# Kernel optimization log

Hardware: AMD Instinct MI355X
Metric: run time of the kernel (lower is better)

The kernel has to match this reference:

```python
import jax, jax.numpy as jnp
import numpy as np

EMBED_DIM = 1024
HEAD_SIZE = 64
BATCH = 8
SEQ = 2048


def setup_inputs() -> dict:
    key = jax.random.key(0)
    k1, k2, k3, k4 = jax.random.split(key, 4)
    x = jax.random.normal(k1, (BATCH, SEQ, EMBED_DIM), dtype=jnp.float32)
    # Dense(use_bias=False) kernels: [in, out]
    scale = 1.0 / np.sqrt(EMBED_DIM)
    Wq = jax.random.normal(k2, (EMBED_DIM, HEAD_SIZE), dtype=jnp.float32) * scale
    Wk = jax.random.normal(k3, (EMBED_DIM, HEAD_SIZE), dtype=jnp.float32) * scale
    Wv = jax.random.normal(k4, (EMBED_DIM, HEAD_SIZE), dtype=jnp.float32) * scale
    return {"x": x, "Wq": Wq, "Wk": Wk, "Wv": Wv}


def reference(x, Wq, Wk, Wv):
    B, S, E = x.shape
    q = jnp.einsum("bse,eh->bsh", x, Wq)
    k = jnp.einsum("bse,eh->bsh", x, Wk)
    v = jnp.einsum("bse,eh->bsh", x, Wv)
    # scores scaled by embedding_dim**-0.5 (as in the original code)
    w = jnp.einsum("bqh,bkh->bqk", q, k) * (E ** -0.5)
    causal = jnp.tril(jnp.ones((S, S), dtype=bool))  # True on/below diag
    w = jnp.where(causal, w, -jnp.inf)
    w = jax.nn.softmax(w, axis=-1)
    # dropout is identity at inference
    return jnp.einsum("bqk,bkh->bqh", w, v)
```

## Files before the change

### kernel.cpp

```cpp
#include <hip/hip_runtime.h>
#include <hip/hip_bf16.h>


#define BATCH 8
#define SEQ   2048
#define EMB   1024
#define HD    64
#define ROWS  (BATCH*SEQ)
#define NTOT  192
#define BK    64
#define NKT   (EMB / BK)

typedef __attribute__((ext_vector_type(8))) short short8;
typedef __attribute__((ext_vector_type(4))) float floatx4;

static __device__ __forceinline__ short f2bf(float f) {
  union { __hip_bfloat16 h; short s; } u;
  u.h = __float2bfloat16(f);
  return u.s;
}

static __device__ __forceinline__ short8 pack8(float4 u, float4 v) {
  short8 r;
  r[0] = f2bf(u.x); r[1] = f2bf(u.y); r[2] = f2bf(u.z); r[3] = f2bf(u.w);
  r[4] = f2bf(v.x); r[5] = f2bf(v.y); r[6] = f2bf(v.z); r[7] = f2bf(v.w);
  return r;
}

static __device__ __forceinline__ void gload_lds16(const void* g, void* l) {
  __builtin_amdgcn_global_load_lds(
      (const __attribute__((address_space(1))) unsigned int*)g,
      (__attribute__((address_space(3))) unsigned int*)l, 16, 0, 0);
}

__global__ __launch_bounds__(256) void wt_kernel(
    const float* __restrict__ Wq, const float* __restrict__ Wk,
    const float* __restrict__ Wv, short* __restrict__ Wts) {
  const int id = blockIdx.x * 256 + threadIdx.x;
  const int kt = id / 1536;
  const int rem = id - kt * 1536;
  const int np = rem >> 3;
  const int s = rem & 7;
  const float* __restrict__ W = (np < 64) ? Wq : ((np < 128) ? Wk : Wv);
  const int n = np & 63;
  const int k0 = kt * BK + (s ^ (np & 7)) * 8;
  short8 o;
#pragma unroll
  for (int u = 0; u < 8; ++u) o[u] = f2bf(W[(size_t)(k0 + u) * HD + n]);
  *(short8*)(Wts + (size_t)id * 8) = o;
}

__global__ __launch_bounds__(256, 2) void proj_kernel(
    const float* __restrict__ x, const short* __restrict__ Wts,
    short* __restrict__ qb, short* __restrict__ kb_, short* __restrict__ vtb) {
  __shared__ __align__(16) float As[32 * 64];
  __shared__ __align__(16) short Bs[192 * 64];

  const int t = threadIdx.x, lane = t & 63, w = t >> 6;
  const int lo = lane & 15, quad = lane >> 4;
  const int e = lo & 7;
  const int m0 = blockIdx.x * 32;

  const int cc0 = w * 2, cc1 = cc0 + 1;
  const int ar0 = cc0 * 4 + (lane >> 4);
  const int ar1 = cc1 * 4 + (lane >> 4);
  const int aj = lane & 15;
  const float* agp0 = x + (size_t)(m0 + ar0) * EMB + ((aj ^ (ar0 & 7)) * 4);
  const float* agp1 = x + (size_t)(m0 + ar1) * EMB + ((aj ^ (ar1 & 7)) * 4);
  float* alp0 = As + cc0 * 256;
  float* alp1 = As + cc1 * 256;

  const short* bgp = Wts + (size_t)(w * 6) * 512 + lane * 8;
  short* blp = Bs + (w * 6) * 512;

  floatx4 acc[2][3];
#pragma unroll
  for (int mf = 0; mf < 2; ++mf)
#pragma unroll
    for (int j = 0; j < 3; ++j) acc[mf][j] = (floatx4){0.f, 0.f, 0.f, 0.f};

  for (int kt = 0; kt < NKT; ++kt) {
    __syncthreads();
    gload_lds16(agp0 + kt * BK, alp0);
    gload_lds16(agp1 + kt * BK, alp1);
    const short* bg = bgp + (size_t)kt * 12288;
#pragma unroll
    for (int i = 0; i < 6; ++i)
      gload_lds16(bg + i * 512, blp + i * 512);
    __syncthreads();

    short8 af[2][2];
#pragma unroll
    for (int mf = 0; mf < 2; ++mf) {
      const float* Ar = As + (mf * 16 + lo) * 64;
#pragma unroll
      for (int ks = 0; ks < 2; ++ks) {
        const float4 f0 = *(const float4*)(Ar + (((8 * ks + 2 * quad) ^ e) << 2));
        const float4 f1 = *(const float4*)(Ar + (((8 * ks + 2 * quad + 1) ^ e) << 2));
        af[mf][ks] = pack8(f0, f1);
      }
    }
    short8 bf[3][2];
#pragma unroll
    for (int j = 0; j < 3; ++j) {
      const short* Br = Bs + ((w * 3 + j) * 16 + lo) * 64;
#pragma unroll
      for (int ks = 0; ks < 2; ++ks)
        bf[j][ks] = *(const short8*)(Br + (((4 * ks + quad) ^ e) << 3));
    }
#pragma unroll
    for (int ks = 0; ks < 2; ++ks)
#pragma unroll
      for (int j = 0; j < 3; ++j) {
        acc[0][j] = __builtin_amdgcn_mfma_f32_16x16x32_bf16(af[0][ks], bf[j][ks], acc[0][j], 0, 0, 0);
        acc[1][j] = __builtin_amdgcn_mfma_f32_16x16x32_bf16(af[1][ks], bf[j][ks], acc[1][j], 0, 0, 0);
      }
  }

  const int bb = m0 >> 11;
  const int sbase = (m0 & (SEQ - 1)) + quad * 4;
#pragma unroll
  for (int mf = 0; mf < 2; ++mf) {
    const int rowb = m0 + mf * 16 + quad * 4;
#pragma unroll
    for (int j = 0; j < 3; ++j) {
      const int nt = w * 3 + j;
      const floatx4 v = acc[mf][j];
      if (nt < 4) {
#pragma unroll
        for (int r = 0; r < 4; ++r)
          qb[(size_t)(rowb + r) * HD + nt * 16 + lo] = f2bf(v[r] * 0.03125f);
      } else if (nt < 8) {
#pragma unroll
        for (int r = 0; r < 4; ++r)
          kb_[(size_t)(rowb + r) * HD + (nt - 4) * 16 + lo] = f2bf(v[r]);
      } else {
        const int col = (nt - 8) * 16 + lo;
        short4 sv = make_short4(f2bf(v[0]), f2bf(v[1]), f2bf(v[2]), f2bf(v[3]));
        *(short4*)(vtb + ((size_t)bb * HD + col) * SEQ + sbase + mf * 16) = sv;
      }
    }
  }
}

#define KSTR 72
#define PSTR 40

__global__ __launch_bounds__(256, 2) void attn_kernel(
    const short* __restrict__ qb, const short* __restrict__ kb,
    const short* __restrict__ vtb, float* __restrict__ out) {
  __shared__ __align__(16) short Ks[2][64 * KSTR];
  __shared__ __align__(16) short Vs[2][64 * KSTR];
  __shared__ __align__(16) short Ps[4][16 * PSTR];
  __shared__ __align__(16) floatx4 Red[2][5][64];

  const int b = blockIdx.y;
  const int bx = blockIdx.x;
  const int qx = (bx & 1) ? (63 - (bx >> 1)) : (bx >> 1);
  const int q0 = qx * 32;
  const int t = threadIdx.x, lane = t & 63, w = t >> 6;
  const int wr = w >> 1, wk = w & 1;
  const int lo = lane & 15, quad = lane >> 4;

  const short* qp = qb + ((size_t)b * SEQ + q0 + wr * 16 + lo) * HD + quad * 8;
  const short8 qf0 = *(const short8*)(qp);
  const short8 qf1 = *(const short8*)(qp + 32);

  const int r0 = t >> 3, c0 = (t & 7) * 8;
  const int r1 = r0 + 32;
  const short* __restrict__ kgb = kb + (size_t)b * SEQ * HD;
  const short* __restrict__ vgb = vtb + (size_t)b * HD * SEQ;

  floatx4 acc[4];
  float lsum[4] = {0.f, 0.f, 0.f, 0.f};
#pragma unroll
  for (int nt = 0; nt < 4; ++nt) acc[nt] = (floatx4){0.f, 0.f, 0.f, 0.f};

  {
    short8 k0v = *(const short8*)(kgb + (size_t)r0 * HD + c0);
    short8 k1v = *(const short8*)(kgb + (size_t)r1 * HD + c0);
    short8 v0v = *(const short8*)(vgb + (size_t)r0 * SEQ + c0);
    short8 v1v = *(const short8*)(vgb + (size_t)r1 * SEQ + c0);
    *(short8*)(&Ks[0][r0 * KSTR + c0]) = k0v;
    *(short8*)(&Ks[0][r1 * KSTR + c0]) = k1v;
    *(short8*)(&Vs[0][r0 * KSTR + c0]) = v0v;
    *(short8*)(&Vs[0][r1 * KSTR + c0]) = v1v;
  }

  const int niter = q0 / 64 + 1;
  for (int it = 0; it < niter; ++it) {
    const int j0 = it * 64;
    const int buf = it & 1;
    __syncthreads();

    short8 kfr[2][2], vfr[4];
#pragma unroll
    for (int n2 = 0; n2 < 2; ++n2) {
      const short* kr = &Ks[buf][(wk * 32 + n2 * 16 + lo) * KSTR + quad * 8];
      kfr[n2][0] = *(const short8*)(kr);
      kfr[n2][1] = *(const short8*)(kr + 32);
    }
#pragma unroll
    for (int nt = 0; nt < 4; ++nt)
      vfr[nt] = *(const short8*)(&Vs[buf][(nt * 16 + lo) * KSTR + wk * 32 + quad * 8]);

    short8 nk0, nk1, nv0, nv1;
    const bool more = (it + 1 < niter);
    if (more) {
      const int jn = j0 + 64;
      nk0 = *(const short8*)(kgb + (size_t)(jn + r0) * HD + c0);
      nk1 = *(const short8*)(kgb + (size_t)(jn + r1) * HD + c0);
      nv0 = *(const short8*)(vgb + (size_t)r0 * SEQ + jn + c0);
      nv1 = *(const short8*)(vgb + (size_t)r1 * SEQ + jn + c0);
    }

    floatx4 s0 = (floatx4){0.f, 0.f, 0.f, 0.f};
    floatx4 s1 = (floatx4){0.f, 0.f, 0.f, 0.f};
    s0 = __builtin_amdgcn_mfma_f32_16x16x32_bf16(qf0, kfr[0][0], s0, 0, 0, 0);
    s0 = __builtin_amdgcn_mfma_f32_16x16x32_bf16(qf1, kfr[0][1], s0, 0, 0, 0);
    s1 = __builtin_amdgcn_mfma_f32_16x16x32_bf16(qf0, kfr[1][0], s1, 0, 0, 0);
    s1 = __builtin_amdgcn_mfma_f32_16x16x32_bf16(qf1, kfr[1][1], s1, 0, 0, 0);

    const bool diag = (j0 + 64 > q0);
    const int rowb = q0 + wr * 16 + quad * 4;
    short* Pw = Ps[w];
#pragma unroll
    for (int r = 0; r < 4; ++r) {
      float e0 = __expf(s0[r]);
      float e1 = __expf(s1[r]);
      if (diag) {
        const int key0 = j0 + wk * 32 + lo;
        e0 = (key0 <= rowb + r) ? e0 : 0.f;
        e1 = (key0 + 16 <= rowb + r) ? e1 : 0.f;
      }
      lsum[r] += e0 + e1;
      Pw[(quad * 4 + r) * PSTR + lo] = f2bf(e0);
      Pw[(quad * 4 + r) * PSTR + 16 + lo] = f2bf(e1);
    }
    const short8 pf = *(const short8*)(&Pw[lo * PSTR + quad * 8]);
#pragma unroll
    for (int nt = 0; nt < 4; ++nt)
      acc[nt] = __builtin_amdgcn_mfma_f32_16x16x32_bf16(pf, vfr[nt], acc[nt], 0, 0, 0);

    if (more) {
      const int nb = buf ^ 1;
      *(short8*)(&Ks[nb][r0 * KSTR + c0]) = nk0;
      *(short8*)(&Ks[nb][r1 * KSTR + c0]) = nk1;
      *(short8*)(&Vs[nb][r0 * KSTR + c0]) = nv0;
      *(short8*)(&Vs[nb][r1 * KSTR + c0]) = nv1;
    }
  }

#pragma unroll
  for (int d = 1; d < 16; d <<= 1) {
#pragma unroll
    for (int r = 0; r < 4; ++r) lsum[r] += __shfl_xor(lsum[r], d);
  }

  if (wk == 1) {
#pragma unroll
    for (int nt = 0; nt < 4; ++nt) Red[wr][nt][lane] = acc[nt];
    Red[wr][4][lane] = (floatx4){lsum[0], lsum[1], lsum[2], lsum[3]};
  }
  __syncthreads();
  if (wk == 0) {
    const floatx4 lp = Red[wr][4][lane];
    const int rowb = q0 + wr * 16 + quad * 4;
#pragma unroll
    for (int nt = 0; nt < 4; ++nt) {
      const floatx4 o = acc[nt] + Red[wr][nt][lane];
#pragma unroll
      for (int r = 0; r < 4; ++r)
        out[((size_t)b * SEQ + rowb + r) * HD + nt * 16 + lo] =
            o[r] / (lsum[r] + lp[r]);
    }
  }
}

extern "C" void kernel_launch(void* const* d_in, const int* in_sizes, int n_in,
                              void* d_out, int out_size, void* d_ws, size_t ws_size,
                              hipStream_t stream) {
  const float* x  = (const float*)d_in[0];
  const float* Wq = (const float*)d_in[1];
  const float* Wk = (const float*)d_in[2];
  const float* Wv = (const float*)d_in[3];
  float* out = (float*)d_out;
  short* ws = (short*)d_ws;
  short* qbp = ws;
  short* kbp = ws + (size_t)ROWS * HD;
  short* vtp = ws + (size_t)2 * ROWS * HD;
  short* Wts = ws + (size_t)3 * ROWS * HD;

  wt_kernel<<<dim3(96), 256, 0, stream>>>(Wq, Wk, Wv, Wts);
  proj_kernel<<<dim3(ROWS / 32), 256, 0, stream>>>(x, Wts, qbp, kbp, vtp);
  attn_kernel<<<dim3(SEQ / 32, BATCH), 256, 0, stream>>>(qbp, kbp, vtp, out);
}
```

Before: 148.8 us.

## Load MFMA fragments directly from global memory and double-buffer projection A tiles

The weight prep kernel now writes weights in MFMA fragment order, so the projection kernel loads B fragments straight into registers instead of staging them through shared memory. The x tile is double-buffered in LDS, which leaves one barrier per k-step. The attention kernel drops its K/V shared-memory staging and ping-pongs register prefetches read straight from global/L2, with s_setprio raised around MFMA sections, and replaces the per-element divide with a reciprocal multiply. This removes LDS traffic and barriers but depends on L2 to absorb the K/V reads repeated across the two wave-rows, and raises register pressure.

```diff
diff --git a/kernel.cpp b/kernel.cpp
--- a/kernel.cpp
+++ b/kernel.cpp
@@ -35,26 +35,28 @@
 
 __global__ __launch_bounds__(256) void wt_kernel(
     const float* __restrict__ Wq, const float* __restrict__ Wk,
-    const float* __restrict__ Wv, short* __restrict__ Wts) {
+    const float* __restrict__ Wv, short* __restrict__ Wd) {
   const int id = blockIdx.x * 256 + threadIdx.x;
-  const int kt = id / 1536;
-  const int rem = id - kt * 1536;
-  const int np = rem >> 3;
-  const int s = rem & 7;
+  const int lane = id & 63;
+  const int ks = (id >> 6) & 1;
+  const int id2 = id >> 7;
+  const int nt = id2 % 12;
+  const int kt = id2 / 12;
+  const int lo = lane & 15, quad = lane >> 4;
+  const int np = nt * 16 + lo;
   const float* __restrict__ W = (np < 64) ? Wq : ((np < 128) ? Wk : Wv);
   const int n = np & 63;
-  const int k0 = kt * BK + (s ^ (np & 7)) * 8;
+  const int k0 = kt * BK + (4 * ks + quad) * 8;
   short8 o;
 #pragma unroll
   for (int u = 0; u < 8; ++u) o[u] = f2bf(W[(size_t)(k0 + u) * HD + n]);
-  *(short8*)(Wts + (size_t)id * 8) = o;
+  *(short8*)(Wd + (size_t)id * 8) = o;
 }
 
 __global__ __launch_bounds__(256, 2) void proj_kernel(
-    const float* __restrict__ x, const short* __restrict__ Wts,
+    const float* __restrict__ x, const short* __restrict__ Wd,
     short* __restrict__ qb, short* __restrict__ kb_, short* __restrict__ vtb) {
-  __shared__ __align__(16) float As[32 * 64];
-  __shared__ __align__(16) short Bs[192 * 64];
+  __shared__ __align__(16) float As[2][32 * 64];
 
   const int t = threadIdx.x, lane = t & 63, w = t >> 6;
   const int lo = lane & 15, quad = lane >> 4;
@@ -62,16 +64,12 @@
   const int m0 = blockIdx.x * 32;
 
   const int cc0 = w * 2, cc1 = cc0 + 1;
-  const int ar0 = cc0 * 4 + (lane >> 4);
-  const int ar1 = cc1 * 4 + (lane >> 4);
-  const int aj = lane & 15;
-  const float* agp0 = x + (size_t)(m0 + ar0) * EMB + ((aj ^ (ar0 & 7)) * 4);
-  const float* agp1 = x + (size_t)(m0 + ar1) * EMB + ((aj ^ (ar1 & 7)) * 4);
-  float* alp0 = As + cc0 * 256;
-  float* alp1 = As + cc1 * 256;
-
-  const short* bgp = Wts + (size_t)(w * 6) * 512 + lane * 8;
-  short* blp = Bs + (w * 6) * 512;
+  const int ar0 = cc0 * 4 + quad;
+  const int ar1 = cc1 * 4 + quad;
+  const float* agp0 = x + (size_t)(m0 + ar0) * EMB + ((lo ^ (ar0 & 7)) * 4);
+  const float* agp1 = x + (size_t)(m0 + ar1) * EMB + ((lo ^ (ar1 & 7)) * 4);
+
+  const short* bgp = Wd + (size_t)(w * 3) * 1024 + lane * 8;
 
   floatx4 acc[2][3];
 #pragma unroll
@@ -79,20 +77,35 @@
 #pragma unroll
     for (int j = 0; j < 3; ++j) acc[mf][j] = (floatx4){0.f, 0.f, 0.f, 0.f};
 
+  short8 bcur[3][2], bnxt[3][2];
+
+  auto STAGE_A = [&](int buf, int kt) {
+    gload_lds16(agp0 + kt * BK, &As[buf][cc0 * 256]);
+    gload_lds16(agp1 + kt * BK, &As[buf][cc1 * 256]);
+  };
+  auto LOAD_B = [&](short8 (&bf)[3][2], int kt) {
+    const short* bg = bgp + (size_t)kt * 12288;
+#pragma unroll
+    for (int j = 0; j < 3; ++j)
+#pragma unroll
+      for (int ks = 0; ks < 2; ++ks)
+        bf[j][ks] = *(const short8*)(bg + j * 1024 + ks * 512);
+  };
+
+  STAGE_A(0, 0);
+  LOAD_B(bcur, 0);
+  int buf = 0;
+#pragma unroll
   for (int kt = 0; kt < NKT; ++kt) {
     __syncthreads();
-    gload_lds16(agp0 + kt * BK, alp0);
-    gload_lds16(agp1 + kt * BK, alp1);
-    const short* bg = bgp + (size_t)kt * 12288;
-#pragma unroll
-    for (int i = 0; i < 6; ++i)
-      gload_lds16(bg + i * 512, blp + i * 512);
-    __syncthreads();
-
+    if (kt + 1 < NKT) {
+      STAGE_A(buf ^ 1, kt + 1);
+      LOAD_B(bnxt, kt + 1);
+    }
     short8 af[2][2];
 #pragma unroll
     for (int mf = 0; mf < 2; ++mf) {
-      const float* Ar = As + (mf * 16 + lo) * 64;
+      const float* Ar = &As[buf][(mf * 16 + lo) * 64];
 #pragma unroll
       for (int ks = 0; ks < 2; ++ks) {
         const float4 f0 = *(const float4*)(Ar + (((8 * ks + 2 * quad) ^ e) << 2));
@@ -100,21 +113,18 @@
         af[mf][ks] = pack8(f0, f1);
       }
     }
-    short8 bf[3][2];
-#pragma unroll
-    for (int j = 0; j < 3; ++j) {
-      const short* Br = Bs + ((w * 3 + j) * 16 + lo) * 64;
-#pragma unroll
-      for (int ks = 0; ks < 2; ++ks)
-        bf[j][ks] = *(const short8*)(Br + (((4 * ks + quad) ^ e) << 3));
-    }
 #pragma unroll
     for (int ks = 0; ks < 2; ++ks)
 #pragma unroll
       for (int j = 0; j < 3; ++j) {
-        acc[0][j] = __builtin_amdgcn_mfma_f32_16x16x32_bf16(af[0][ks], bf[j][ks], acc[0][j], 0, 0, 0);
-        acc[1][j] = __builtin_amdgcn_mfma_f32_16x16x32_bf16(af[1][ks], bf[j][ks], acc[1][j], 0, 0, 0);
-      }
+        acc[0][j] = __builtin_amdgcn_mfma_f32_16x16x32_bf16(af[0][ks], bcur[j][ks], acc[0][j], 0, 0, 0);
+        acc[1][j] = __builtin_amdgcn_mfma_f32_16x16x32_bf16(af[1][ks], bcur[j][ks], acc[1][j], 0, 0, 0);
+      }
+#pragma unroll
+    for (int j = 0; j < 3; ++j)
+#pragma unroll
+      for (int ks = 0; ks < 2; ++ks) bcur[j][ks] = bnxt[j][ks];
+    buf ^= 1;
   }
 
   const int bb = m0 >> 11;
@@ -143,14 +153,11 @@
   }
 }
 
-#define KSTR 72
 #define PSTR 40
 
 __global__ __launch_bounds__(256, 2) void attn_kernel(
     const short* __restrict__ qb, const short* __restrict__ kb,
     const short* __restrict__ vtb, float* __restrict__ out) {
-  __shared__ __align__(16) short Ks[2][64 * KSTR];
-  __shared__ __align__(16) short Vs[2][64 * KSTR];
   __shared__ __align__(16) short Ps[4][16 * PSTR];
   __shared__ __align__(16) floatx4 Red[2][5][64];
 
@@ -166,64 +173,43 @@
   const short8 qf0 = *(const short8*)(qp);
   const short8 qf1 = *(const short8*)(qp + 32);
 
-  const int r0 = t >> 3, c0 = (t & 7) * 8;
-  const int r1 = r0 + 32;
   const short* __restrict__ kgb = kb + (size_t)b * SEQ * HD;
   const short* __restrict__ vgb = vtb + (size_t)b * HD * SEQ;
+  const short* kbase = kgb + (size_t)(wk * 32 + lo) * HD + quad * 8;
+  const short* vbase = vgb + (size_t)lo * SEQ + wk * 32 + quad * 8;
 
   floatx4 acc[4];
   float lsum[4] = {0.f, 0.f, 0.f, 0.f};
 #pragma unroll
   for (int nt = 0; nt < 4; ++nt) acc[nt] = (floatx4){0.f, 0.f, 0.f, 0.f};
 
-  {
-    short8 k0v = *(const short8*)(kgb + (size_t)r0 * HD + c0);
-    short8 k1v = *(const short8*)(kgb + (size_t)r1 * HD + c0);
-    short8 v0v = *(const short8*)(vgb + (size_t)r0 * SEQ + c0);
-    short8 v1v = *(const short8*)(vgb + (size_t)r1 * SEQ + c0);
-    *(short8*)(&Ks[0][r0 * KSTR + c0]) = k0v;
-    *(short8*)(&Ks[0][r1 * KSTR + c0]) = k1v;
-    *(short8*)(&Vs[0][r0 * KSTR + c0]) = v0v;
-    *(short8*)(&Vs[0][r1 * KSTR + c0]) = v1v;
-  }
-
-  const int niter = q0 / 64 + 1;
-  for (int it = 0; it < niter; ++it) {
-    const int j0 = it * 64;
-    const int buf = it & 1;
-    __syncthreads();
-
-    short8 kfr[2][2], vfr[4];
+  auto LOAD = [&](short8 (&kf)[2][2], short8 (&vf)[4], int j0) {
+    const short* kp = kbase + (size_t)j0 * HD;
 #pragma unroll
     for (int n2 = 0; n2 < 2; ++n2) {
-      const short* kr = &Ks[buf][(wk * 32 + n2 * 16 + lo) * KSTR + quad * 8];
-      kfr[n2][0] = *(const short8*)(kr);
-      kfr[n2][1] = *(const short8*)(kr + 32);
-    }
+      kf[n2][0] = *(const short8*)(kp + n2 * (16 * HD));
+      kf[n2][1] = *(const short8*)(kp + n2 * (16 * HD) + 32);
+    }
+    const short* vp = vbase + j0;
 #pragma unroll
     for (int nt = 0; nt < 4; ++nt)
-      vfr[nt] = *(const short8*)(&Vs[buf][(nt * 16 + lo) * KSTR + wk * 32 + quad * 8]);
-
-    short8 nk0, nk1, nv0, nv1;
-    const bool more = (it + 1 < niter);
-    if (more) {
-      const int jn = j0 + 64;
-      nk0 = *(const short8*)(kgb + (size_t)(jn + r0) * HD + c0);
-      nk1 = *(const short8*)(kgb + (size_t)(jn + r1) * HD + c0);
-      nv0 = *(const short8*)(vgb + (size_t)r0 * SEQ + jn + c0);
-      nv1 = *(const short8*)(vgb + (size_t)r1 * SEQ + jn + c0);
-    }
-
+      vf[nt] = *(const short8*)(vp + (size_t)(nt * 16) * SEQ);
+  };
+
+  short* Pw = Ps[w];
+  const int rowb = q0 + wr * 16 + quad * 4;
+
+  auto STEP = [&](short8 (&kf)[2][2], short8 (&vf)[4], int j0) {
     floatx4 s0 = (floatx4){0.f, 0.f, 0.f, 0.f};
     floatx4 s1 = (floatx4){0.f, 0.f, 0.f, 0.f};
-    s0 = __builtin_amdgcn_mfma_f32_16x16x32_bf16(qf0, kfr[0][0], s0, 0, 0, 0);
-    s0 = __builtin_amdgcn_mfma_f32_16x16x32_bf16(qf1, kfr[0][1], s0, 0, 0, 0);
-    s1 = __builtin_amdgcn_mfma_f32_16x16x32_bf16(qf0, kfr[1][0], s1, 0, 0, 0);
-    s1 = __builtin_amdgcn_mfma_f32_16x16x32_bf16(qf1, kfr[1][1], s1, 0, 0, 0);
+    __builtin_amdgcn_s_setprio(1);
+    s0 = __builtin_amdgcn_mfma_f32_16x16x32_bf16(qf0, kf[0][0], s0, 0, 0, 0);
+    s0 = __builtin_amdgcn_mfma_f32_16x16x32_bf16(qf1, kf[0][1], s0, 0, 0, 0);
+    s1 = __builtin_amdgcn_mfma_f32_16x16x32_bf16(qf0, kf[1][0], s1, 0, 0, 0);
+    s1 = __builtin_amdgcn_mfma_f32_16x16x32_bf16(qf1, kf[1][1], s1, 0, 0, 0);
+    __builtin_amdgcn_s_setprio(0);
 
     const bool diag = (j0 + 64 > q0);
-    const int rowb = q0 + wr * 16 + quad * 4;
-    short* Pw = Ps[w];
 #pragma unroll
     for (int r = 0; r < 4; ++r) {
       float e0 = __expf(s0[r]);
@@ -238,17 +224,24 @@
       Pw[(quad * 4 + r) * PSTR + 16 + lo] = f2bf(e1);
     }
     const short8 pf = *(const short8*)(&Pw[lo * PSTR + quad * 8]);
+    __builtin_amdgcn_s_setprio(1);
 #pragma unroll
     for (int nt = 0; nt < 4; ++nt)
-      acc[nt] = __builtin_amdgcn_mfma_f32_16x16x32_bf16(pf, vfr[nt], acc[nt], 0, 0, 0);
-
-    if (more) {
-      const int nb = buf ^ 1;
-      *(short8*)(&Ks[nb][r0 * KSTR + c0]) = nk0;
-      *(short8*)(&Ks[nb][r1 * KSTR + c0]) = nk1;
-      *(short8*)(&Vs[nb][r0 * KSTR + c0]) = nv0;
-      *(short8*)(&Vs[nb][r1 * KSTR + c0]) = nv1;
-    }
+      acc[nt] = __builtin_amdgcn_mfma_f32_16x16x32_bf16(pf, vf[nt], acc[nt], 0, 0, 0);
+    __builtin_amdgcn_s_setprio(0);
+  };
+
+  const int niter = q0 / 64 + 1;
+  short8 kA[2][2], vA[4], kB[2][2], vB[4];
+  LOAD(kA, vA, 0);
+  int it = 0;
+  while (true) {
+    if (it + 1 < niter) LOAD(kB, vB, (it + 1) * 64);
+    STEP(kA, vA, it * 64);
+    ++it; if (it >= niter) break;
+    if (it + 1 < niter) LOAD(kA, vA, (it + 1) * 64);
+    STEP(kB, vB, it * 64);
+    ++it; if (it >= niter) break;
   }
 
 #pragma unroll
@@ -265,14 +258,15 @@
   __syncthreads();
   if (wk == 0) {
     const floatx4 lp = Red[wr][4][lane];
-    const int rowb = q0 + wr * 16 + quad * 4;
+    float invd[4];
+#pragma unroll
+    for (int r = 0; r < 4; ++r) invd[r] = 1.0f / (lsum[r] + lp[r]);
 #pragma unroll
     for (int nt = 0; nt < 4; ++nt) {
       const floatx4 o = acc[nt] + Red[wr][nt][lane];
 #pragma unroll
       for (int r = 0; r < 4; ++r)
-        out[((size_t)b * SEQ + rowb + r) * HD + nt * 16 + lo] =
-            o[r] / (lsum[r] + lp[r]);
+        out[((size_t)b * SEQ + rowb + r) * HD + nt * 16 + lo] = o[r] * invd[r];
     }
   }
 }
@@ -289,9 +283,9 @@
   short* qbp = ws;
   short* kbp = ws + (size_t)ROWS * HD;
   short* vtp = ws + (size_t)2 * ROWS * HD;
-  short* Wts = ws + (size_t)3 * ROWS * HD;
-
-  wt_kernel<<<dim3(96), 256, 0, stream>>>(Wq, Wk, Wv, Wts);
-  proj_kernel<<<dim3(ROWS / 32), 256, 0, stream>>>(x, Wts, qbp, kbp, vtp);
+  short* Wd  = ws + (size_t)3 * ROWS * HD;
+
+  wt_kernel<<<dim3(96), 256, 0, stream>>>(Wq, Wk, Wv, Wd);
+  proj_kernel<<<dim3(ROWS / 32), 256, 0, stream>>>(x, Wd, qbp, kbp, vtp);
   attn_kernel<<<dim3(SEQ / 32, BATCH), 256, 0, stream>>>(qbp, kbp, vtp, out);
 }
```

After: 175.6 us. 18.0% more time.
